# Optimization experiments

Hardware: AMD Instinct MI355X
Metric: run time of the kernel (lower is better)

Reference implementation:

```python
import jax, jax.numpy as jnp
from jax import lax
import numpy as np

B, T, D, H, O = 128, 256, 512, 1024, 1024


def setup_inputs() -> dict:
    key = jax.random.key(0)
    ks = jax.random.split(key, 6)
    s = 0.02
    x = jax.random.normal(ks[0], (B, T, D), dtype=jnp.float32)
    # Gates stacked in order (i, f, g, o). Each gate in the original has three
    # biases (W_x*.bias + W_h*.bias + b_*); their sum is equivalent to the
    # single per-gate bias b below (same function space).
    Wx = jax.random.normal(ks[1], (4, H, D), dtype=jnp.float32) * s
    Wh = jax.random.normal(ks[2], (4, H, H), dtype=jnp.float32) * s
    b = jax.random.normal(ks[3], (4, H), dtype=jnp.float32) * s
    Whp = jax.random.normal(ks[4], (O, H), dtype=jnp.float32) * s
    bhp = jax.random.normal(ks[5], (O,), dtype=jnp.float32) * s
    return {"x": x, "Wx": Wx, "Wh": Wh, "b": b, "Whp": Whp, "bhp": bhp}


def reference(x, Wx, Wh, b, Whp, bhp):
    batch = x.shape[0]
    hid = Wh.shape[-1]
    # Precompute all input projections in one big GEMM: [B,T,4,H]
    xproj = jnp.einsum('btd,ghd->btgh', x, Wx) + b

    def step(carry, xp_t):
        h, c = carry
        # xp_t: [B,4,H]; recurrent projection for all 4 gates in one GEMM
        gates = xp_t + jnp.einsum('bk,gok->bgo', h, Wh)
        i_t = jax.nn.sigmoid(gates[:, 0])
        f_t = jax.nn.sigmoid(gates[:, 1])
        g_t = jnp.tanh(gates[:, 2])
        o_t = jax.nn.sigmoid(gates[:, 3])
        c = f_t * c + i_t * g_t
        h = o_t * jnp.tanh(c)
        return (h, c), None

    h0 = jnp.zeros((batch, hid), dtype=x.dtype)
    c0 = jnp.zeros((batch, hid), dtype=x.dtype)
    (h_T, _), _ = lax.scan(step, (h0, c0), jnp.swapaxes(xproj, 0, 1))
    logits = h_T @ Whp.T + bhp
    return jax.nn.softmax(logits, axis=1)
```

## Files before the change

kernel.cpp:

```cpp
#include <hip/hip_runtime.h>

#define B_ 128
#define T_ 256
#define D_ 512
#define H_ 1024
#define O_ 1024
#define NWG 256
#define NCOL 32

typedef _Float16 f16;
typedef _Float16 f16x8 __attribute__((ext_vector_type(8)));
typedef float f32x4 __attribute__((ext_vector_type(4)));

#define HSTEP 131072ull

#define OFF_XH   0ull
#define SZ_XH    33554432ull
#define OFF_WHPK (OFF_XH + SZ_XH)
#define SZ_WHPK  8388608ull
#define OFF_WXPK (OFF_WHPK + SZ_WHPK)
#define SZ_WXPK  4194304ull
#define OFF_BIAS (OFF_WXPK + SZ_WXPK)
#define SZ_BIAS  16384ull
#define OFF_H    (OFF_BIAS + SZ_BIAS)
#define SZ_H     (2ull * HSTEP * (T_ + 1))
#define OFF_WHPT (OFF_H + SZ_H)
#define SZ_WHPT  4194304ull
#define OFF_BAR  (OFF_WHPT + SZ_WHPT)

__device__ __forceinline__ void st_h16(f16* p, f16x8 v)
{
    asm volatile("global_store_dwordx4 %0, %1, off sc0 sc1"
                 :: "v"(p), "v"(v) : "memory");
}

__device__ __forceinline__ int ld_flag(const int* p)
{
    int r;
    asm volatile("global_load_dword %0, %1, off sc0 sc1\n\t"
                 "s_waitcnt vmcnt(0)"
                 : "=v"(r) : "v"(p) : "memory");
    return r;
}


__global__ __launch_bounds__(256, 1)
void pack_x(const float* __restrict__ x, f16* __restrict__ xh)
{
    const int id = blockIdx.x * 256 + threadIdx.x;
    const int doct = id & 63;
    const int t = (id >> 6) & 255;
    const int b = id >> 14;
    const float* src = x + ((size_t)b * T_ + t) * D_ + (doct << 3);
    const float4 v0 = *(const float4*)src;
    const float4 v1 = *(const float4*)(src + 4);
    f16x8 o;
    o[0] = (f16)v0.x; o[1] = (f16)v0.y; o[2] = (f16)v0.z; o[3] = (f16)v0.w;
    o[4] = (f16)v1.x; o[5] = (f16)v1.y; o[6] = (f16)v1.z; o[7] = (f16)v1.w;
    *(f16x8*)(xh + ((((size_t)t << 6) + doct) * B_ + b) * 8) = o;
}

__global__ __launch_bounds__(256, 1)
void pack_wh(const float* __restrict__ Wh, f16* __restrict__ whpk)
{
    const int id = blockIdx.x * 256 + threadIdx.x;
    const int n = id & 31;
    const int koct = (id >> 5) & 127;
    const int w = id >> 12;
    const int g = n >> 3;
    const int o = (w << 3) + (n & 7);
    const float* src = Wh + ((size_t)g * H_ + o) * H_ + (koct << 3);
    const float4 v0 = *(const float4*)src;
    const float4 v1 = *(const float4*)(src + 4);
    f16x8 ov;
    ov[0] = (f16)v0.x; ov[1] = (f16)v0.y; ov[2] = (f16)v0.z; ov[3] = (f16)v0.w;
    ov[4] = (f16)v1.x; ov[5] = (f16)v1.y; ov[6] = (f16)v1.z; ov[7] = (f16)v1.w;
    *(f16x8*)(whpk + (size_t)id * 8) = ov;
}

__global__ __launch_bounds__(256, 1)
void pack_wx(const float* __restrict__ Wx, f16* __restrict__ wxpk)
{
    const int id = blockIdx.x * 256 + threadIdx.x;
    const int n = id & 31;
    const int doct = (id >> 5) & 63;
    const int w = id >> 11;
    const int g = n >> 3;
    const int o = (w << 3) + (n & 7);
    const float* src = Wx + ((size_t)g * H_ + o) * D_ + (doct << 3);
    const float4 v0 = *(const float4*)src;
    const float4 v1 = *(const float4*)(src + 4);
    f16x8 ov;
    ov[0] = (f16)v0.x; ov[1] = (f16)v0.y; ov[2] = (f16)v0.z; ov[3] = (f16)v0.w;
    ov[4] = (f16)v1.x; ov[5] = (f16)v1.y; ov[6] = (f16)v1.z; ov[7] = (f16)v1.w;
    *(f16x8*)(wxpk + (size_t)id * 8) = ov;
}

__global__ __launch_bounds__(256, 1)
void pack_bias(const float* __restrict__ bsrc, float* __restrict__ biasp)
{
    const int id = blockIdx.x * 256 + threadIdx.x;
    const int n = id & 31;
    const int w = id >> 5;
    biasp[id] = bsrc[((size_t)(n >> 3) << 10) + (w << 3) + (n & 7)];
}

__global__ __launch_bounds__(256, 1)
void whp_t(const float* __restrict__ Whp, float* __restrict__ wT)
{
    __shared__ float tile[64][65];
    const int bx = blockIdx.x & 15;
    const int by = blockIdx.x >> 4;
    for (int i = threadIdx.x; i < 4096; i += 256) {
        const int r = i >> 6, c = i & 63;
        tile[r][c] = Whp[((size_t)(by * 64 + r) << 10) + bx * 64 + c];
    }
    __syncthreads();
    for (int i = threadIdx.x; i < 4096; i += 256) {
        const int r = i >> 6, c = i & 63;
        wT[((size_t)(bx * 64 + r) << 10) + by * 64 + c] = tile[c][r];
    }
}

__global__ __launch_bounds__(512, 1)
void lstm_loop(const f16* __restrict__ xh,
               const f16* __restrict__ whpk,
               const f16* __restrict__ wxpk,
               const float* __restrict__ biasp,
               f16* __restrict__ hbuf,
               int* __restrict__ bar)
{
    __shared__ f16   lds_wh[(H_/8) * NCOL * 8];
    __shared__ f16   lds_wx[(D_/8) * NCOL * 8];
    __shared__ float lds_red[4][8][64];
    __shared__ f16   lds_hst[64 * 8];

    const int tid = threadIdx.x;
    const int w = blockIdx.x;
    const int dom = w >> 7;
    const int wc = w & 127;

    {
        const f16x8* s1 = (const f16x8*)(whpk + (size_t)wc * (H_/8) * NCOL * 8);
        f16x8* d1 = (f16x8*)lds_wh;
        for (int i = tid; i < (H_/8) * NCOL; i += 512) d1[i] = s1[i];
        const f16x8* s2 = (const f16x8*)(wxpk + (size_t)wc * (D_/8) * NCOL * 8);
        f16x8* d2 = (f16x8*)lds_wx;
        for (int i = tid; i < (D_/8) * NCOL; i += 512) d2[i] = s2[i];
    }
    __syncthreads();

    const int lane = tid & 63;
    const int wv = tid >> 6;
    const int kb = wv >> 2;
    const int rg = wv & 3;
    const int quad = lane >> 4;
    const int l16 = lane & 15;
    const int mrow = (dom << 6) + (rg << 4) + l16;

    const float b0r = biasp[wc * NCOL + l16];
    const float b1r = biasp[wc * NCOL + 16 + l16];
    const float i0 = kb ? b0r : 0.f;
    const float i1 = kb ? b1r : 0.f;

    float cs0 = 0.f, cs1 = 0.f;
    const int hi = (l16 >> 3) & 1;
    const int r0 = hi << 1;
    const int oc = l16 & 7;
    const int rowbase = (rg << 4) + (quad << 2) + r0;

    const int* __restrict__ fbase = bar + (dom << 7) + (kb << 6);

    for (int t = 0; t < T_; ++t) {
        const f16* __restrict__ hr = hbuf + (size_t)t * HSTEP;
        f16* hw = hbuf + (size_t)(t + 1) * HSTEP;

        f32x4 acc0 = {i0, i0, i0, i0};
        f32x4 acc1 = {i1, i1, i1, i1};

        const f16* __restrict__ xt = xh + (size_t)t * (D_/8) * B_ * 8;
        {
            f16x8 XA[8];
            #pragma unroll
            for (int kc = 0; kc < 8; ++kc) {
                const int koct = (kb << 5) + (kc << 2) + quad;
                XA[kc] = *(const f16x8*)(xt + (((size_t)koct << 7) + mrow) * 8);
            }
            #pragma unroll
            for (int kc = 0; kc < 8; ++kc) {
                const int koct = (kb << 5) + (kc << 2) + quad;
                f16x8 b0 = *(const f16x8*)(lds_wx + ((koct << 5) + l16) * 8);
                f16x8 b1 = *(const f16x8*)(lds_wx + ((koct << 5) + 16 + l16) * 8);
                acc0 = __builtin_amdgcn_mfma_f32_16x16x32_f16(XA[kc], b0, acc0, 0, 0, 0);
                acc1 = __builtin_amdgcn_mfma_f32_16x16x32_f16(XA[kc], b1, acc1, 0, 0, 0);
            }
        }

        if (t) {
            const int* f0 = fbase + lane;
            while (!__all(ld_flag(f0) >= t))
                __builtin_amdgcn_s_sleep(1);
        }

        {
            f16x8 A[16];
            #pragma unroll
            for (int kc = 0; kc < 16; ++kc) {
                const int koct = (kb << 6) + (kc << 2) + quad;
                A[kc] = *(const f16x8*)(hr + (((size_t)koct << 7) + mrow) * 8);
            }
            #pragma unroll
            for (int kc = 0; kc < 16; ++kc) {
                const int koct = (kb << 6) + (kc << 2) + quad;
                f16x8 b0 = *(const f16x8*)(lds_wh + ((koct << 5) + l16) * 8);
                f16x8 b1 = *(const f16x8*)(lds_wh + ((koct << 5) + 16 + l16) * 8);
                acc0 = __builtin_amdgcn_mfma_f32_16x16x32_f16(A[kc], b0, acc0, 0, 0, 0);
                acc1 = __builtin_amdgcn_mfma_f32_16x16x32_f16(A[kc], b1, acc1, 0, 0, 0);
            }
        }

        if (!kb) {
            #pragma unroll
            for (int r = 0; r < 4; ++r) {
                lds_red[rg][r][lane]     = acc0[r];
                lds_red[rg][4 + r][lane] = acc1[r];
            }
        }
        __syncthreads();

        if (kb) {
            #pragma unroll
            for (int r = 0; r < 4; ++r) {
                acc0[r] += lds_red[rg][r][lane];
                acc1[r] += lds_red[rg][4 + r][lane];
            }
            f32x4 p0, p1;
            #pragma unroll
            for (int r = 0; r < 4; ++r) {
                p0[r] = __shfl_xor(acc0[r], 8, 64);
                p1[r] = __shfl_xor(acc1[r], 8, 64);
            }
            #pragma unroll
            for (int i = 0; i < 2; ++i) {
                const int r = r0 + i;
                const float gi = hi ? p0[r]   : acc0[r];
                const float gf = hi ? acc0[r] : p0[r];
                const float gg = hi ? p1[r]   : acc1[r];
                const float go = hi ? acc1[r] : p1[r];
                const float it = 1.0f / (1.0f + __expf(-gi));
                const float ft = 1.0f / (1.0f + __expf(-gf));
                const float eg = __expf(2.0f * gg);
                const float gt = 1.0f - 2.0f / (eg + 1.0f);
                const float ot = 1.0f / (1.0f + __expf(-go));
                float c = (i == 0) ? cs0 : cs1;
                c = ft * c + it * gt;
                if (i == 0) cs0 = c; else cs1 = c;
                const float ec = __expf(2.0f * c);
                const float tc = 1.0f - 2.0f / (ec + 1.0f);
                lds_hst[((rowbase + i) << 3) + oc] = (f16)(ot * tc);
            }
        }
        __syncthreads();

        if (tid < 64) {
            f16x8 v = *(const f16x8*)(lds_hst + (tid << 3));
            st_h16(hw + ((size_t)(wc << 7) + (dom << 6) + tid) * 8, v);
            asm volatile("s_waitcnt vmcnt(0)" ::: "memory");
        }
        __syncthreads();
        if (tid == 0)
            __hip_atomic_store(bar + w, t + 1, __ATOMIC_RELAXED, __HIP_MEMORY_SCOPE_AGENT);
    }
}

__global__ __launch_bounds__(256, 1)
void finale(const f16* __restrict__ hT,
            const float* __restrict__ whpT,
            const float* __restrict__ bhp,
            float* __restrict__ outp)
{
    __shared__ float hrow[H_];
    __shared__ float red[16];
    const int tid = threadIdx.x;
    const int b = blockIdx.x;

    if (tid < H_/8) {
        f16x8 v = *(const f16x8*)(hT + (((size_t)tid << 7) + b) * 8);
        #pragma unroll
        for (int j = 0; j < 8; ++j) hrow[(tid << 3) + j] = (float)v[j];
    }
    __syncthreads();

    float lg0 = bhp[tid], lg1 = bhp[tid + 256], lg2 = bhp[tid + 512], lg3 = bhp[tid + 768];
    for (int k = 0; k < H_; ++k) {
        const float hv = hrow[k];
        const float* wr = whpT + ((size_t)k << 10);
        lg0 = fmaf(hv, wr[tid],       lg0);
        lg1 = fmaf(hv, wr[tid + 256], lg1);
        lg2 = fmaf(hv, wr[tid + 512], lg2);
        lg3 = fmaf(hv, wr[tid + 768], lg3);
    }

    const int lane = tid & 63, wv = tid >> 6;
    float mx = fmaxf(fmaxf(lg0, lg1), fmaxf(lg2, lg3));
    for (int off = 32; off > 0; off >>= 1) mx = fmaxf(mx, __shfl_down(mx, off, 64));
    if (lane == 0) red[wv] = mx;
    __syncthreads();
    mx = fmaxf(fmaxf(red[0], red[1]), fmaxf(red[2], red[3]));

    const float e0 = __expf(lg0 - mx), e1 = __expf(lg1 - mx);
    const float e2 = __expf(lg2 - mx), e3 = __expf(lg3 - mx);
    float s = e0 + e1 + e2 + e3;
    for (int off = 32; off > 0; off >>= 1) s += __shfl_down(s, off, 64);
    if (lane == 0) red[8 + wv] = s;
    __syncthreads();
    s = red[8] + red[9] + red[10] + red[11];
    const float inv = 1.0f / s;

    float* op = outp + ((size_t)b << 10);
    op[tid]       = e0 * inv;
    op[tid + 256] = e1 * inv;
    op[tid + 512] = e2 * inv;
    op[tid + 768] = e3 * inv;
}

extern "C" void kernel_launch(void* const* d_in, const int* in_sizes, int n_in,
                              void* d_out, int out_size, void* d_ws, size_t ws_size,
                              hipStream_t stream)
{
    const float* x    = (const float*)d_in[0];
    const float* Wx   = (const float*)d_in[1];
    const float* Wh   = (const float*)d_in[2];
    const float* bias = (const float*)d_in[3];
    const float* Whp  = (const float*)d_in[4];
    const float* bhp  = (const float*)d_in[5];

    char* ws = (char*)d_ws;
    f16*   xh    = (f16*)(ws + OFF_XH);
    f16*   whpk  = (f16*)(ws + OFF_WHPK);
    f16*   wxpk  = (f16*)(ws + OFF_WXPK);
    float* biasp = (float*)(ws + OFF_BIAS);
    f16*   hbuf  = (f16*)(ws + OFF_H);
    float* whpT  = (float*)(ws + OFF_WHPT);
    int*   bar   = (int*)(ws + OFF_BAR);

    hipMemsetAsync(ws + OFF_H, 0, 2ull * HSTEP, stream);
    hipMemsetAsync(ws + OFF_BAR, 0, 1024, stream);

    pack_x   <<<8192, 256, 0, stream>>>(x, xh);
    pack_wh  <<<2048, 256, 0, stream>>>(Wh, whpk);
    pack_wx  <<<1024, 256, 0, stream>>>(Wx, wxpk);
    pack_bias<<<16,   256, 0, stream>>>(bias, biasp);
    whp_t    <<<256,  256, 0, stream>>>(Whp, whpT);

    lstm_loop<<<NWG, 512, 0, stream>>>(xh, whpk, wxpk, biasp, hbuf, bar);
    finale   <<<B_,  256, 0, stream>>>(hbuf + (size_t)T_ * HSTEP, whpT, bhp, (float*)d_out);
}
```

Measured before the change: 1.466 ms.

## Split LSTM step K-reduction across four wave groups with 1024-thread blocks

Doubles the lstm_loop block to 1024 threads and splits both the input and recurrent K dimensions into four quarters instead of two. Three quarters write partial sums to LDS and the last one reduces and applies the gate nonlinearities. Each wave group now polls only the 32 barrier flags that cover its own K slice. The per-step flag store is moved inside the tid<64 block, which drops one __syncthreads. The aim is to cut the serial MFMA chain per wave on the critical path of each timestep. In exchange it adds more LDS reduction traffic, larger blocks and register pressure limited to a 1024-thread launch bound.

Result: faster. 1.204 ms (-17.9%).

```diff
diff --git a/kernel.cpp b/kernel.cpp
--- a/kernel.cpp
+++ b/kernel.cpp
@@ -122,7 +122,7 @@
     }
 }
 
-__global__ __launch_bounds__(512, 1)
+__global__ __launch_bounds__(1024, 1)
 void lstm_loop(const f16* __restrict__ xh,
                const f16* __restrict__ whpk,
                const f16* __restrict__ wxpk,
@@ -132,7 +132,7 @@
 {
     __shared__ f16   lds_wh[(H_/8) * NCOL * 8];
     __shared__ f16   lds_wx[(D_/8) * NCOL * 8];
-    __shared__ float lds_red[4][8][64];
+    __shared__ float lds_red[3][4][8][64];
     __shared__ f16   lds_hst[64 * 8];
 
     const int tid = threadIdx.x;
@@ -143,25 +143,26 @@
     {
         const f16x8* s1 = (const f16x8*)(whpk + (size_t)wc * (H_/8) * NCOL * 8);
         f16x8* d1 = (f16x8*)lds_wh;
-        for (int i = tid; i < (H_/8) * NCOL; i += 512) d1[i] = s1[i];
+        for (int i = tid; i < (H_/8) * NCOL; i += 1024) d1[i] = s1[i];
         const f16x8* s2 = (const f16x8*)(wxpk + (size_t)wc * (D_/8) * NCOL * 8);
         f16x8* d2 = (f16x8*)lds_wx;
-        for (int i = tid; i < (D_/8) * NCOL; i += 512) d2[i] = s2[i];
+        for (int i = tid; i < (D_/8) * NCOL; i += 1024) d2[i] = s2[i];
     }
     __syncthreads();
 
     const int lane = tid & 63;
     const int wv = tid >> 6;
-    const int kb = wv >> 2;
+    const int kq = wv >> 2;
     const int rg = wv & 3;
     const int quad = lane >> 4;
     const int l16 = lane & 15;
     const int mrow = (dom << 6) + (rg << 4) + l16;
+    const int last = (kq == 3);
 
     const float b0r = biasp[wc * NCOL + l16];
     const float b1r = biasp[wc * NCOL + 16 + l16];
-    const float i0 = kb ? b0r : 0.f;
-    const float i1 = kb ? b1r : 0.f;
+    const float i0 = last ? b0r : 0.f;
+    const float i1 = last ? b1r : 0.f;
 
     float cs0 = 0.f, cs1 = 0.f;
     const int hi = (l16 >> 3) & 1;
@@ -169,7 +170,7 @@
     const int oc = l16 & 7;
     const int rowbase = (rg << 4) + (quad << 2) + r0;
 
-    const int* __restrict__ fbase = bar + (dom << 7) + (kb << 6);
+    const int* __restrict__ fq = bar + (dom << 7) + (kq << 5) + (lane & 31);
 
     for (int t = 0; t < T_; ++t) {
         const f16* __restrict__ hr = hbuf + (size_t)t * HSTEP;
@@ -180,38 +181,37 @@
 
         const f16* __restrict__ xt = xh + (size_t)t * (D_/8) * B_ * 8;
         {
-            f16x8 XA[8];
-            #pragma unroll
-            for (int kc = 0; kc < 8; ++kc) {
-                const int koct = (kb << 5) + (kc << 2) + quad;
-                XA[kc] = *(const f16x8*)(xt + (((size_t)koct << 7) + mrow) * 8);
-            }
-            #pragma unroll
-            for (int kc = 0; kc < 8; ++kc) {
-                const int koct = (kb << 5) + (kc << 2) + quad;
-                f16x8 b0 = *(const f16x8*)(lds_wx + ((koct << 5) + l16) * 8);
-                f16x8 b1 = *(const f16x8*)(lds_wx + ((koct << 5) + 16 + l16) * 8);
+            f16x8 XA[4];
+            #pragma unroll
+            for (int kc = 0; kc < 4; ++kc) {
+                const int doct = (kq << 4) + (kc << 2) + quad;
+                XA[kc] = *(const f16x8*)(xt + (((size_t)doct << 7) + mrow) * 8);
+            }
+            #pragma unroll
+            for (int kc = 0; kc < 4; ++kc) {
+                const int doct = (kq << 4) + (kc << 2) + quad;
+                f16x8 b0 = *(const f16x8*)(lds_wx + ((doct << 5) + l16) * 8);
+                f16x8 b1 = *(const f16x8*)(lds_wx + ((doct << 5) + 16 + l16) * 8);
                 acc0 = __builtin_amdgcn_mfma_f32_16x16x32_f16(XA[kc], b0, acc0, 0, 0, 0);
                 acc1 = __builtin_amdgcn_mfma_f32_16x16x32_f16(XA[kc], b1, acc1, 0, 0, 0);
             }
         }
 
         if (t) {
-            const int* f0 = fbase + lane;
-            while (!__all(ld_flag(f0) >= t))
+            while (!__all(ld_flag(fq) >= t))
                 __builtin_amdgcn_s_sleep(1);
         }
 
         {
-            f16x8 A[16];
-            #pragma unroll
-            for (int kc = 0; kc < 16; ++kc) {
-                const int koct = (kb << 6) + (kc << 2) + quad;
+            f16x8 A[8];
+            #pragma unroll
+            for (int kc = 0; kc < 8; ++kc) {
+                const int koct = (kq << 5) + (kc << 2) + quad;
                 A[kc] = *(const f16x8*)(hr + (((size_t)koct << 7) + mrow) * 8);
             }
             #pragma unroll
-            for (int kc = 0; kc < 16; ++kc) {
-                const int koct = (kb << 6) + (kc << 2) + quad;
+            for (int kc = 0; kc < 8; ++kc) {
+                const int koct = (kq << 5) + (kc << 2) + quad;
                 f16x8 b0 = *(const f16x8*)(lds_wh + ((koct << 5) + l16) * 8);
                 f16x8 b1 = *(const f16x8*)(lds_wh + ((koct << 5) + 16 + l16) * 8);
                 acc0 = __builtin_amdgcn_mfma_f32_16x16x32_f16(A[kc], b0, acc0, 0, 0, 0);
@@ -219,20 +219,23 @@
             }
         }
 
-        if (!kb) {
+        if (!last) {
             #pragma unroll
             for (int r = 0; r < 4; ++r) {
-                lds_red[rg][r][lane]     = acc0[r];
-                lds_red[rg][4 + r][lane] = acc1[r];
+                lds_red[kq][rg][r][lane]     = acc0[r];
+                lds_red[kq][rg][4 + r][lane] = acc1[r];
             }
         }
         __syncthreads();
 
-        if (kb) {
-            #pragma unroll
-            for (int r = 0; r < 4; ++r) {
-                acc0[r] += lds_red[rg][r][lane];
-                acc1[r] += lds_red[rg][4 + r][lane];
+        if (last) {
+            #pragma unroll
+            for (int q = 0; q < 3; ++q) {
+                #pragma unroll
+                for (int r = 0; r < 4; ++r) {
+                    acc0[r] += lds_red[q][rg][r][lane];
+                    acc1[r] += lds_red[q][rg][4 + r][lane];
+                }
             }
             f32x4 p0, p1;
             #pragma unroll
@@ -266,10 +269,9 @@
             f16x8 v = *(const f16x8*)(lds_hst + (tid << 3));
             st_h16(hw + ((size_t)(wc << 7) + (dom << 6) + tid) * 8, v);
             asm volatile("s_waitcnt vmcnt(0)" ::: "memory");
-        }
-        __syncthreads();
-        if (tid == 0)
-            __hip_atomic_store(bar + w, t + 1, __ATOMIC_RELAXED, __HIP_MEMORY_SCOPE_AGENT);
+            if (tid == 0)
+                __hip_atomic_store(bar + w, t + 1, __ATOMIC_RELAXED, __HIP_MEMORY_SCOPE_AGENT);
+        }
     }
 }
 
@@ -353,6 +355,6 @@
     pack_bias<<<16,   256, 0, stream>>>(bias, biasp);
     whp_t    <<<256,  256, 0, stream>>>(Whp, whpT);
 
-    lstm_loop<<<NWG, 512, 0, stream>>>(xh, whpk, wxpk, biasp, hbuf, bar);
+    lstm_loop<<<NWG, 1024, 0, stream>>>(xh, whpk, wxpk, biasp, hbuf, bar);
     finale   <<<B_,  256, 0, stream>>>(hbuf + (size_t)T_ * HSTEP, whpT, bhp, (float*)d_out);
 }
```
